# Performance work log

Hardware: AMD Instinct MI355X
Metric: run time of the kernel (lower is better)

The kernel has to match this reference:

```python
import jax, jax.numpy as jnp
import numpy as np

N_CLASSES = 5
N_SAMPLES = 512
D_EMB = 512


def setup_inputs() -> dict:
    key = jax.random.key(0)
    k1, k2, k3 = jax.random.split(key, 3)
    prediction = jax.random.normal(k1, (N_SAMPLES, D_EMB), dtype=jnp.float32)
    target = jax.random.randint(k2, (N_SAMPLES,), 0, N_CLASSES)
    # learnable_map=None -> all learnable, init = inverse_softplus(0.5 + 0.5*U[0,1))
    t = 0.5 + 0.5 * jax.random.uniform(k3, (N_CLASSES - 1,), dtype=jnp.float32)
    distances_raw = jnp.log(jnp.exp(t) - 1.0)  # inverse softplus (t < 20 always)
    return {"prediction": prediction, "distances_raw": distances_raw, "target": target}


def reference(prediction, distances_raw, target):
    n = prediction.shape[0]
    eps = 1e-8  # torch F.cosine_similarity eps
    xn = prediction / jnp.maximum(jnp.linalg.norm(prediction, axis=1, keepdims=True), eps)
    cos = xn @ xn.T  # [i, j] pairwise cosine similarity

    same = target[:, None] == target[None, :]          # label_diff <= 0
    positives = same & ~jnp.eye(n, dtype=bool)          # same label, not self
    negatives = ~same                                   # different label

    # ordinal class positions from softplus-parameterized gaps
    pos_d = jax.nn.softplus(distances_raw)
    class_pos = jnp.concatenate([jnp.zeros(1, dtype=pos_d.dtype), jnp.cumsum(pos_d)])
    cp = class_pos[target]
    margins = jnp.where(negatives, jnp.abs(cp[:, None] - cp[None, :]), 0.0)  # [i, j]

    # Original loop over anchor-positive columns k:
    #   n_pair_loss[k][i, j] = -cos[i, k] + cos[i, j] + margins[i, j]
    #   valid iff positives[i, k] and negatives[i, j]; invalid -> relu(-inf)=0
    base = cos + margins                                # [i, j]
    diff = base[:, None, :] - cos[:, :, None]           # [i, k, j]
    val = jnp.where(negatives[:, None, :], jax.nn.relu(diff), 0.0)
    s = jnp.where(positives, val.sum(axis=2), 0.0)      # [i, k]
    negcount = negatives.sum(axis=1)                    # [i]
    cnt = jnp.where(positives, negcount[:, None], 0)    # loss_mask2
    L = s / jnp.maximum(cnt, 1)                         # per (anchor i, positive k)

    # mean over nonzero entries (mean_n_pair_loss[mean_n_pair_loss != 0].mean())
    nz = (L != 0.0).sum()
    return L.sum() / jnp.maximum(nz, 1).astype(L.dtype)
```

## Files before the change

### kernel.cpp

```cpp
#include <hip/hip_runtime.h>
#include <math.h>

#define NS 512
#define DE 512
#define NCL 5
#define KSPLIT 4

__global__ __launch_bounds__(256) void k_gemm(const float* __restrict__ pred,
                                              float* __restrict__ part,
                                              float* __restrict__ gsum,
                                              unsigned int* __restrict__ gnz,
                                              unsigned int* __restrict__ ticket) {
    const int tid = threadIdx.x;
    if (blockIdx.x == 0 && blockIdx.y == 0 && blockIdx.z == 0 && tid == 0) {
        *gsum = 0.0f; *gnz = 0u; *ticket = 0u;
    }

    __shared__ float As[16][68];
    __shared__ float Bs[16][68];

    const int tx = tid & 15, ty = tid >> 4;
    const int row0 = blockIdx.y * 64, col0 = blockIdx.x * 64;
    const int kz0 = blockIdx.z * (DE / KSPLIT);
    const int lr = tid >> 2;
    const int lc = (tid & 3) * 4;

    float c[4][4] = {};

    for (int kb = 0; kb < DE / KSPLIT; kb += 16) {
        float4 av = *(const float4*)&pred[(row0 + lr) * DE + kz0 + kb + lc];
        float4 bv = *(const float4*)&pred[(col0 + lr) * DE + kz0 + kb + lc];
        __syncthreads();
        As[lc + 0][lr] = av.x; As[lc + 1][lr] = av.y;
        As[lc + 2][lr] = av.z; As[lc + 3][lr] = av.w;
        Bs[lc + 0][lr] = bv.x; Bs[lc + 1][lr] = bv.y;
        Bs[lc + 2][lr] = bv.z; Bs[lc + 3][lr] = bv.w;
        __syncthreads();
#pragma unroll
        for (int kk = 0; kk < 16; kk++) {
            float4 a = *(const float4*)&As[kk][ty * 4];
            float4 b = *(const float4*)&Bs[kk][tx * 4];
            c[0][0] = fmaf(a.x, b.x, c[0][0]); c[0][1] = fmaf(a.x, b.y, c[0][1]);
            c[0][2] = fmaf(a.x, b.z, c[0][2]); c[0][3] = fmaf(a.x, b.w, c[0][3]);
            c[1][0] = fmaf(a.y, b.x, c[1][0]); c[1][1] = fmaf(a.y, b.y, c[1][1]);
            c[1][2] = fmaf(a.y, b.z, c[1][2]); c[1][3] = fmaf(a.y, b.w, c[1][3]);
            c[2][0] = fmaf(a.z, b.x, c[2][0]); c[2][1] = fmaf(a.z, b.y, c[2][1]);
            c[2][2] = fmaf(a.z, b.z, c[2][2]); c[2][3] = fmaf(a.z, b.w, c[2][3]);
            c[3][0] = fmaf(a.w, b.x, c[3][0]); c[3][1] = fmaf(a.w, b.y, c[3][1]);
            c[3][2] = fmaf(a.w, b.z, c[3][2]); c[3][3] = fmaf(a.w, b.w, c[3][3]);
        }
    }

    float* outp = part + (size_t)blockIdx.z * NS * NS;
#pragma unroll
    for (int m = 0; m < 4; m++) {
        float4 o = make_float4(c[m][0], c[m][1], c[m][2], c[m][3]);
        *(float4*)&outp[(row0 + ty * 4 + m) * NS + col0 + tx * 4] = o;
    }
}

__global__ __launch_bounds__(256) void k_loss(const float* __restrict__ part,
                                              const int* __restrict__ target,
                                              const float* __restrict__ draw,
                                              float* __restrict__ gsum,
                                              unsigned int* __restrict__ gnz,
                                              unsigned int* __restrict__ ticket,
                                              float* __restrict__ out) {
    const int i = blockIdx.x;
    const int tid = threadIdx.x;

    __shared__ float rn[NS];
    __shared__ float v[NS];
    __shared__ float ck[NS];
    __shared__ int   pk[NS];
    __shared__ float redf[256];
    __shared__ int   redi[256];
    __shared__ unsigned int pcount;

    const float* p0 = part;
    const float* p1 = part + NS * NS;
    const float* p2 = part + 2 * NS * NS;
    const float* p3 = part + 3 * NS * NS;

#pragma unroll
    for (int jj = 0; jj < 2; jj++) {
        int j = tid + jj * 256;
        float nsq = p0[j * NS + j] + p1[j * NS + j] + p2[j * NS + j] + p3[j * NS + j];
        rn[j] = 1.0f / fmaxf(sqrtf(nsq), 1e-8f);
    }
    if (tid == 0) pcount = 0u;

    float cp[NCL];
    cp[0] = 0.0f;
#pragma unroll
    for (int c = 0; c < NCL - 1; c++) cp[c + 1] = cp[c] + log1pf(expf(draw[c]));
    const int ti = target[i];
    const float cpi = cp[ti];
    __syncthreads();

    const float rni = rn[i];
    int ncnt = 0;
#pragma unroll
    for (int jj = 0; jj < 2; jj++) {
        int j = tid + jj * 256;
        int tj = target[j];
        float g = p0[i * NS + j] + p1[i * NS + j] + p2[i * NS + j] + p3[i * NS + j];
        float c = g * rni * rn[j];
        ck[j] = c;
        bool neg = (tj != ti);
        v[j] = neg ? (c + fabsf(cpi - cp[tj])) : -1e30f;
        ncnt += neg ? 1 : 0;
        if (!neg && j != i) {
            pk[atomicAdd(&pcount, 1u)] = j;
        }
    }
    redi[tid] = ncnt;
    __syncthreads();
    for (int s = 128; s > 0; s >>= 1) {
        if (tid < s) redi[tid] += redi[tid + s];
        __syncthreads();
    }
    const int negcount = redi[0];
    const unsigned int npos = pcount;
    __syncthreads();

    float ssum = 0.0f;
    int nzc = 0;
    const float4* v4 = (const float4*)v;
    for (unsigned int p = tid; p < npos; p += 256) {
        const float c_k = ck[pk[p]];
        float s0 = 0.0f, s1 = 0.0f;
#pragma unroll 4
        for (int jq = 0; jq < NS / 4; jq++) {
            float4 w = v4[jq];
            s0 += fmaxf(w.x - c_k, 0.0f) + fmaxf(w.y - c_k, 0.0f);
            s1 += fmaxf(w.z - c_k, 0.0f) + fmaxf(w.w - c_k, 0.0f);
        }
        float s = s0 + s1;
        ssum += s;
        if (s != 0.0f) nzc++;
    }

    redf[tid] = ssum;
    redi[tid] = nzc;
    __syncthreads();
    for (int s = 128; s > 0; s >>= 1) {
        if (tid < s) { redf[tid] += redf[tid + s]; redi[tid] += redi[tid + s]; }
        __syncthreads();
    }
    if (tid == 0) {
        int denom = negcount > 1 ? negcount : 1;
        if (redf[0] != 0.0f || redi[0] != 0) {
            atomicAdd(gsum, redf[0] / (float)denom);
            atomicAdd(gnz, (unsigned int)redi[0]);
        }
        __threadfence();
        unsigned int t = atomicAdd(ticket, 1u);
        if (t == (unsigned int)(gridDim.x - 1)) {
            float s = atomicAdd(gsum, 0.0f);
            unsigned int n = atomicAdd(gnz, 0u);
            out[0] = s / (float)(n > 1u ? n : 1u);
        }
    }
}

extern "C" void kernel_launch(void* const* d_in, const int* in_sizes, int n_in,
                              void* d_out, int out_size, void* d_ws, size_t ws_size,
                              hipStream_t stream) {
    const float* pred   = (const float*)d_in[0];
    const float* draw   = (const float*)d_in[1];
    const int*   target = (const int*)d_in[2];
    float* out = (float*)d_out;

    float* ws   = (float*)d_ws;
    float* part = ws;
    float* gsum = ws + KSPLIT * NS * NS;
    unsigned int* gnz    = (unsigned int*)(gsum + 1);
    unsigned int* ticket = (unsigned int*)(gsum + 2);

    hipLaunchKernelGGL(k_gemm, dim3(8, 8, KSPLIT), dim3(256), 0, stream,
                       pred, part, gsum, gnz, ticket);
    hipLaunchKernelGGL(k_loss, dim3(NS), dim3(256), 0, stream,
                       part, target, draw, gsum, gnz, ticket, out);
}
```

Baseline: 94.24 us.

## Split norm kernel, retile GEMM to 128x128 with split-K 16, parallelize loss over columns

Row norms now come from a separate kernel instead of the GEMM diagonals. The GEMM is retiled to 128x128 output blocks with 8x8 register tiles, an XOR-swizzled shared-memory layout and split-K of 16, so each block loads its whole K slice once. The loss kernel now splits the positive-by-negative hinge sum across 16 column groups held in registers, so all threads work even when there are few positives, and reduces the partials through shared memory. In exchange, the workspace grows to 16 partial cosine matrices that the loss kernel must read back, and a third kernel launch is added.

```diff
diff --git a/kernel.cpp b/kernel.cpp
--- a/kernel.cpp
+++ b/kernel.cpp
@@ -4,91 +4,111 @@
 #define NS 512
 #define DE 512
 #define NCL 5
-#define KSPLIT 4
-
-__global__ __launch_bounds__(256) void k_gemm(const float* __restrict__ pred,
-                                              float* __restrict__ part,
-                                              float* __restrict__ gsum,
-                                              unsigned int* __restrict__ gnz,
-                                              unsigned int* __restrict__ ticket) {
+#define KSPLIT 16
+#define PART_ELEMS (KSPLIT * NS * NS)
+
+__global__ __launch_bounds__(256) void k_norm(const float* __restrict__ pred,
+                                              float* __restrict__ rn,
+                                              float* __restrict__ ctrl) {
     const int tid = threadIdx.x;
-    if (blockIdx.x == 0 && blockIdx.y == 0 && blockIdx.z == 0 && tid == 0) {
-        *gsum = 0.0f; *gnz = 0u; *ticket = 0u;
-    }
-
-    __shared__ float As[16][68];
-    __shared__ float Bs[16][68];
+    if (blockIdx.x == 0 && tid == 0) { ctrl[0] = 0.0f; ctrl[1] = 0.0f; ctrl[2] = 0.0f; }
+    const int w = tid >> 6, lane = tid & 63;
+    const float4* p4 = (const float4*)pred;
+#pragma unroll
+    for (int rr = 0; rr < 2; rr++) {
+        const int r = blockIdx.x * 8 + w * 2 + rr;
+        float4 a = p4[r * (DE / 4) + lane];
+        float4 b = p4[r * (DE / 4) + 64 + lane];
+        float ss = a.x * a.x + a.y * a.y + a.z * a.z + a.w * a.w
+                 + b.x * b.x + b.y * b.y + b.z * b.z + b.w * b.w;
+#pragma unroll
+        for (int m = 32; m >= 1; m >>= 1) ss += __shfl_xor(ss, m, 64);
+        if (lane == 0) rn[r] = 1.0f / fmaxf(sqrtf(ss), 1e-8f);
+    }
+}
+
+__global__ __launch_bounds__(256, 1) void k_gemm(const float* __restrict__ pred,
+                                                 float* __restrict__ part) {
+    __shared__ float4 As4[128][8];
+    __shared__ float4 Bs4[128][8];
+
+    const int tid = threadIdx.x;
+    const int row0 = blockIdx.y * 128, col0 = blockIdx.x * 128;
+    const int kz0 = blockIdx.z * 32;
+
+    const int lr = tid >> 1;
+    const int sbase = (tid & 1) * 4;
+    const int swz = (lr >> 3) & 7;
+    const float4* gA = (const float4*)&pred[(row0 + lr) * DE + kz0];
+    const float4* gB = (const float4*)&pred[(col0 + lr) * DE + kz0];
+#pragma unroll
+    for (int q = 0; q < 4; q++) {
+        int s = sbase + q;
+        As4[lr][s ^ swz] = gA[s];
+        Bs4[lr][s ^ swz] = gB[s];
+    }
+    __syncthreads();
 
     const int tx = tid & 15, ty = tid >> 4;
-    const int row0 = blockIdx.y * 64, col0 = blockIdx.x * 64;
-    const int kz0 = blockIdx.z * (DE / KSPLIT);
-    const int lr = tid >> 2;
-    const int lc = (tid & 3) * 4;
-
-    float c[4][4] = {};
-
-    for (int kb = 0; kb < DE / KSPLIT; kb += 16) {
-        float4 av = *(const float4*)&pred[(row0 + lr) * DE + kz0 + kb + lc];
-        float4 bv = *(const float4*)&pred[(col0 + lr) * DE + kz0 + kb + lc];
-        __syncthreads();
-        As[lc + 0][lr] = av.x; As[lc + 1][lr] = av.y;
-        As[lc + 2][lr] = av.z; As[lc + 3][lr] = av.w;
-        Bs[lc + 0][lr] = bv.x; Bs[lc + 1][lr] = bv.y;
-        Bs[lc + 2][lr] = bv.z; Bs[lc + 3][lr] = bv.w;
-        __syncthreads();
-#pragma unroll
-        for (int kk = 0; kk < 16; kk++) {
-            float4 a = *(const float4*)&As[kk][ty * 4];
-            float4 b = *(const float4*)&Bs[kk][tx * 4];
-            c[0][0] = fmaf(a.x, b.x, c[0][0]); c[0][1] = fmaf(a.x, b.y, c[0][1]);
-            c[0][2] = fmaf(a.x, b.z, c[0][2]); c[0][3] = fmaf(a.x, b.w, c[0][3]);
-            c[1][0] = fmaf(a.y, b.x, c[1][0]); c[1][1] = fmaf(a.y, b.y, c[1][1]);
-            c[1][2] = fmaf(a.y, b.z, c[1][2]); c[1][3] = fmaf(a.y, b.w, c[1][3]);
-            c[2][0] = fmaf(a.z, b.x, c[2][0]); c[2][1] = fmaf(a.z, b.y, c[2][1]);
-            c[2][2] = fmaf(a.z, b.z, c[2][2]); c[2][3] = fmaf(a.z, b.w, c[2][3]);
-            c[3][0] = fmaf(a.w, b.x, c[3][0]); c[3][1] = fmaf(a.w, b.y, c[3][1]);
-            c[3][2] = fmaf(a.w, b.z, c[3][2]); c[3][3] = fmaf(a.w, b.w, c[3][3]);
-        }
-    }
-
-    float* outp = part + (size_t)blockIdx.z * NS * NS;
-#pragma unroll
-    for (int m = 0; m < 4; m++) {
-        float4 o = make_float4(c[m][0], c[m][1], c[m][2], c[m][3]);
-        *(float4*)&outp[(row0 + ty * 4 + m) * NS + col0 + tx * 4] = o;
-    }
-}
-
-__global__ __launch_bounds__(256) void k_loss(const float* __restrict__ part,
-                                              const int* __restrict__ target,
-                                              const float* __restrict__ draw,
-                                              float* __restrict__ gsum,
-                                              unsigned int* __restrict__ gnz,
-                                              unsigned int* __restrict__ ticket,
-                                              float* __restrict__ out) {
+    const int aswz = ty & 7, bswz = tx & 7;
+    float acc[8][8] = {};
+
+#pragma unroll
+    for (int q = 0; q < 8; q++) {
+        float4 b4[8];
+#pragma unroll
+        for (int c = 0; c < 8; c++) b4[c] = Bs4[tx * 8 + c][q ^ bswz];
+#pragma unroll
+        for (int rr = 0; rr < 2; rr++) {
+            float4 a4[4];
+#pragma unroll
+            for (int r = 0; r < 4; r++) a4[r] = As4[ty * 8 + rr * 4 + r][q ^ aswz];
+#pragma unroll
+            for (int r = 0; r < 4; r++) {
+#pragma unroll
+                for (int c = 0; c < 8; c++) {
+                    float v = acc[rr * 4 + r][c];
+                    v = fmaf(a4[r].x, b4[c].x, v);
+                    v = fmaf(a4[r].y, b4[c].y, v);
+                    v = fmaf(a4[r].z, b4[c].z, v);
+                    v = fmaf(a4[r].w, b4[c].w, v);
+                    acc[rr * 4 + r][c] = v;
+                }
+            }
+        }
+    }
+
+    float* op = part + (size_t)blockIdx.z * NS * NS;
+#pragma unroll
+    for (int m = 0; m < 8; m++) {
+        float4 o0 = make_float4(acc[m][0], acc[m][1], acc[m][2], acc[m][3]);
+        float4 o1 = make_float4(acc[m][4], acc[m][5], acc[m][6], acc[m][7]);
+        float* dst = &op[(row0 + ty * 8 + m) * NS + col0 + tx * 8];
+        *(float4*)dst = o0;
+        *(float4*)(dst + 4) = o1;
+    }
+}
+
+__global__ __launch_bounds__(256, 2) void k_loss(const float* __restrict__ part,
+                                                 const float* __restrict__ rn,
+                                                 const int* __restrict__ target,
+                                                 const float* __restrict__ draw,
+                                                 float* __restrict__ ctrl,
+                                                 float* __restrict__ out) {
     const int i = blockIdx.x;
     const int tid = threadIdx.x;
 
-    __shared__ float rn[NS];
-    __shared__ float v[NS];
-    __shared__ float ck[NS];
-    __shared__ int   pk[NS];
-    __shared__ float redf[256];
-    __shared__ int   redi[256];
+    __shared__ float4 v4s[NS / 4];
+    __shared__ float  ck[NS];
+    __shared__ int    pk[NS];
+    __shared__ float  spart[NS * 17];
+    __shared__ float  redf[256];
+    __shared__ int    redi[256];
     __shared__ unsigned int pcount;
 
-    const float* p0 = part;
-    const float* p1 = part + NS * NS;
-    const float* p2 = part + 2 * NS * NS;
-    const float* p3 = part + 3 * NS * NS;
-
-#pragma unroll
-    for (int jj = 0; jj < 2; jj++) {
-        int j = tid + jj * 256;
-        float nsq = p0[j * NS + j] + p1[j * NS + j] + p2[j * NS + j] + p3[j * NS + j];
-        rn[j] = 1.0f / fmaxf(sqrtf(nsq), 1e-8f);
-    }
-    if (tid == 0) pcount = 0u;
+    float* gsum = ctrl;
+    unsigned int* gnz    = (unsigned int*)(ctrl + 1);
+    unsigned int* ticket = (unsigned int*)(ctrl + 2);
 
     float cp[NCL];
     cp[0] = 0.0f;
@@ -96,24 +116,30 @@
     for (int c = 0; c < NCL - 1; c++) cp[c + 1] = cp[c] + log1pf(expf(draw[c]));
     const int ti = target[i];
     const float cpi = cp[ti];
-    __syncthreads();
-
     const float rni = rn[i];
-    int ncnt = 0;
-#pragma unroll
-    for (int jj = 0; jj < 2; jj++) {
-        int j = tid + jj * 256;
-        int tj = target[j];
-        float g = p0[i * NS + j] + p1[i * NS + j] + p2[i * NS + j] + p3[i * NS + j];
-        float c = g * rni * rn[j];
-        ck[j] = c;
-        bool neg = (tj != ti);
-        v[j] = neg ? (c + fabsf(cpi - cp[tj])) : -1e30f;
-        ncnt += neg ? 1 : 0;
-        if (!neg && j != i) {
-            pk[atomicAdd(&pcount, 1u)] = j;
-        }
-    }
+    if (tid == 0) pcount = 0u;
+    __syncthreads();
+
+    float2 g = make_float2(0.0f, 0.0f);
+#pragma unroll
+    for (int z = 0; z < KSPLIT; z++) {
+        float2 t = ((const float2*)&part[(size_t)z * NS * NS + (size_t)i * NS])[tid];
+        g.x += t.x; g.y += t.y;
+    }
+    const int j0 = tid * 2;
+    float2 rnj = ((const float2*)rn)[tid];
+    float c0 = g.x * rni * rnj.x;
+    float c1 = g.y * rni * rnj.y;
+    int tj0 = target[j0], tj1 = target[j0 + 1];
+    bool n0 = (tj0 != ti), n1 = (tj1 != ti);
+    ck[j0] = c0; ck[j0 + 1] = c1;
+    float2 vv = make_float2(n0 ? (c0 + fabsf(cpi - cp[tj0])) : -1e30f,
+                            n1 ? (c1 + fabsf(cpi - cp[tj1])) : -1e30f);
+    ((float2*)v4s)[tid] = vv;
+    int ncnt = (n0 ? 1 : 0) + (n1 ? 1 : 0);
+    if (!n0 && j0 != i)     pk[atomicAdd(&pcount, 1u)] = j0;
+    if (!n1 && j0 + 1 != i) pk[atomicAdd(&pcount, 1u)] = j0 + 1;
+
     redi[tid] = ncnt;
     __syncthreads();
     for (int s = 128; s > 0; s >>= 1) {
@@ -124,19 +150,30 @@
     const unsigned int npos = pcount;
     __syncthreads();
 
+    const int kl = tid & 15, jc = tid >> 4;
+    float4 vj[8];
+#pragma unroll
+    for (int t = 0; t < 8; t++) vj[t] = v4s[jc * 8 + t];
+
+    for (unsigned int p = kl; p < npos; p += 16) {
+        const float ckp = ck[pk[p]];
+        float s0 = 0.0f, s1 = 0.0f;
+#pragma unroll
+        for (int t = 0; t < 8; t++) {
+            float4 w = vj[t];
+            s0 += fmaxf(w.x - ckp, 0.0f) + fmaxf(w.y - ckp, 0.0f);
+            s1 += fmaxf(w.z - ckp, 0.0f) + fmaxf(w.w - ckp, 0.0f);
+        }
+        spart[p * 17 + jc] = s0 + s1;
+    }
+    __syncthreads();
+
     float ssum = 0.0f;
     int nzc = 0;
-    const float4* v4 = (const float4*)v;
     for (unsigned int p = tid; p < npos; p += 256) {
-        const float c_k = ck[pk[p]];
-        float s0 = 0.0f, s1 = 0.0f;
-#pragma unroll 4
-        for (int jq = 0; jq < NS / 4; jq++) {
-            float4 w = v4[jq];
-            s0 += fmaxf(w.x - c_k, 0.0f) + fmaxf(w.y - c_k, 0.0f);
-            s1 += fmaxf(w.z - c_k, 0.0f) + fmaxf(w.w - c_k, 0.0f);
-        }
-        float s = s0 + s1;
+        float s = 0.0f;
+#pragma unroll
+        for (int q = 0; q < 16; q++) s += spart[p * 17 + q];
         ssum += s;
         if (s != 0.0f) nzc++;
     }
@@ -174,12 +211,11 @@
 
     float* ws   = (float*)d_ws;
     float* part = ws;
-    float* gsum = ws + KSPLIT * NS * NS;
-    unsigned int* gnz    = (unsigned int*)(gsum + 1);
-    unsigned int* ticket = (unsigned int*)(gsum + 2);
-
-    hipLaunchKernelGGL(k_gemm, dim3(8, 8, KSPLIT), dim3(256), 0, stream,
-                       pred, part, gsum, gnz, ticket);
+    float* rn   = ws + PART_ELEMS;
+    float* ctrl = ws + PART_ELEMS + NS;
+
+    hipLaunchKernelGGL(k_norm, dim3(64), dim3(256), 0, stream, pred, rn, ctrl);
+    hipLaunchKernelGGL(k_gemm, dim3(4, 4, KSPLIT), dim3(256), 0, stream, pred, part);
     hipLaunchKernelGGL(k_loss, dim3(NS), dim3(256), 0, stream,
-                       part, target, draw, gsum, gnz, ticket, out);
-}
+                       part, rn, target, draw, ctrl, out);
+}
```

After: 98.49 us. 4.5% more time.
